# Kernel tuning notes

Hardware: AMD Instinct MI355X
Metric: run time of the kernel (lower is better)

Reference implementation:

```python
import jax, jax.numpy as jnp
import numpy as np

N = 160000          # n_users + n_entities (amazon-book scale)
E = 5_120_000       # nonzeros in A_in (avg degree 32)
DIMS = [64, 64, 32, 16]  # conv_dim_list 64-32-16 on top of embed_dim 64


def setup_inputs() -> dict:
    key = jax.random.key(0)
    ks = jax.random.split(key, 4 + 4 * (len(DIMS) - 1))
    inp = {
        "ego": jax.random.normal(ks[0], (N, DIMS[0]), dtype=jnp.float32) * 0.1,
        "edge_row": jax.random.randint(ks[1], (E,), 0, N, dtype=jnp.int32),
        "edge_col": jax.random.randint(ks[2], (E,), 0, N, dtype=jnp.int32),
        # normalized-adjacency-like values
        "edge_val": jax.random.uniform(ks[3], (E,), dtype=jnp.float32) / 32.0,
    }
    ki = 4
    for i in range(len(DIMS) - 1):
        din, dout = DIMS[i], DIMS[i + 1]
        scale = 1.0 / np.sqrt(din)
        inp[f"W1_{i}"] = jax.random.normal(ks[ki], (din, dout), dtype=jnp.float32) * scale
        inp[f"b1_{i}"] = jnp.zeros((dout,), dtype=jnp.float32)
        inp[f"W2_{i}"] = jax.random.normal(ks[ki + 1], (din, dout), dtype=jnp.float32) * scale
        inp[f"b2_{i}"] = jnp.zeros((dout,), dtype=jnp.float32)
        ki += 2
    return inp


def _leaky(x):
    return jnp.where(x >= 0, x, 0.01 * x)  # nn.LeakyReLU default slope


def _l2norm(x):
    # F.normalize(x, p=2, dim=1), eps=1e-12
    n = jnp.sqrt(jnp.sum(x * x, axis=1, keepdims=True))
    return x / jnp.maximum(n, 1e-12)


def _spmm(row, col, val, x):
    # sparse A_in (COO) @ x : gather neighbor rows, scale, scatter-add
    msgs = val[:, None] * x[col]                      # [E, d]
    return jax.ops.segment_sum(msgs, row, num_segments=N)  # [N, d]


def reference(ego, edge_row, edge_col, edge_val,
              W1_0, b1_0, W2_0, b2_0,
              W1_1, b1_1, W2_1, b2_1,
              W1_2, b1_2, W2_2, b2_2):
    params = [(W1_0, b1_0, W2_0, b2_0),
              (W1_1, b1_1, W2_1, b2_1),
              (W1_2, b1_2, W2_2, b2_2)]
    x = ego
    all_embed = [x]
    for W1, b1, W2, b2 in params:
        side = _spmm(edge_row, edge_col, edge_val, x)         # A_in @ ego
        sum_emb = _leaky((x + side) @ W1 + b1)                # linear1 branch
        bi_emb = _leaky((x * side) @ W2 + b2)                 # linear2 branch
        x = sum_emb + bi_emb                                  # (dropout = identity, eval)
        all_embed.append(_l2norm(x))
    return jnp.concatenate(all_embed, axis=1)                 # [N, 64+64+32+16]
```

## Files before the change

kernel.cpp:

```cpp
#include <hip/hip_runtime.h>
#include <hip/hip_bf16.h>

#define LEAKY(v) ((v) >= 0.0f ? (v) : 0.01f * (v))

typedef int iv4 __attribute__((ext_vector_type(4)));
typedef unsigned short us4 __attribute__((ext_vector_type(4)));
typedef short s8v __attribute__((ext_vector_type(8)));
typedef float f4 __attribute__((ext_vector_type(4)));
typedef float fv8 __attribute__((ext_vector_type(8)));
typedef unsigned uv8 __attribute__((ext_vector_type(8)));

constexpr int SH = 9;
constexpr int RPB = 1 << SH;
constexpr int NBMAX = 320;
constexpr int CHUNK = 6144;

__device__ __forceinline__ unsigned short f2bf(float v) {
  unsigned u = __float_as_uint(v);
  return (unsigned short)((u + 0x7fffu + ((u >> 16) & 1u)) >> 16);
}
__device__ __forceinline__ float bf2f(unsigned short h) {
  return __uint_as_float((unsigned)h << 16);
}

__global__ void k_init(const float* __restrict__ ego, float* __restrict__ out,
                       unsigned short* __restrict__ xh, int n) {
  int tid = blockIdx.x * blockDim.x + threadIdx.x;
  int total = n * 16;
  int stride = gridDim.x * blockDim.x;
  for (int t = tid; t < total; t += stride) {
    int r = t >> 4, c = (t & 15) * 4;
    float4 v = *(const float4*)(ego + (size_t)r * 64 + c);
    *(float4*)(out + (size_t)r * 176 + c) = v;
    if (xh) {
      us4 h;
      h.x = f2bf(v.x); h.y = f2bf(v.y); h.z = f2bf(v.z); h.w = f2bf(v.w);
      *(us4*)(xh + (size_t)r * 64 + c) = h;
    }
  }
}

__global__ void __launch_bounds__(256) k_hist(const int* __restrict__ erow,
                                              int* __restrict__ bcnt, int E, int nb) {
  __shared__ int h[NBMAX];
  for (int i = threadIdx.x; i < NBMAX; i += 256) h[i] = 0;
  __syncthreads();
  int tid = blockIdx.x * blockDim.x + threadIdx.x;
  int stride = gridDim.x * blockDim.x;
  for (int e = tid; e < E; e += stride) atomicAdd(&h[erow[e] >> SH], 1);
  __syncthreads();
  for (int b = threadIdx.x; b < nb; b += 256)
    if (h[b]) atomicAdd(&bcnt[b], h[b]);
}

__global__ void k_scanb(const int* __restrict__ bcnt, int* __restrict__ boff,
                        int* __restrict__ bcur, int* __restrict__ rp,
                        int nb, int n, int E) {
  int l = threadIdx.x;
  constexpr int PB = NBMAX / 64;
  int local[PB];
  int s = 0;
  int base = l * PB;
  for (int j = 0; j < PB; ++j) {
    int b = base + j;
    int c = (b < nb) ? bcnt[b] : 0;
    local[j] = c;
    s += c;
  }
  int incl = s;
  for (int d = 1; d < 64; d <<= 1) {
    int v = __shfl_up(incl, d);
    if (l >= d) incl += v;
  }
  int ex = incl - s;
  for (int j = 0; j < PB; ++j) {
    int b = base + j;
    if (b <= nb) { boff[b] = ex; bcur[b] = ex; }
    ex += local[j];
  }
  if (l == 63) boff[nb] = incl;
  if (l == 0) rp[n] = E;
}

__global__ void __launch_bounds__(256) k_bucket(
    const int* __restrict__ erow, const int* __restrict__ ecol,
    const float* __restrict__ ev, int* __restrict__ bcur,
    int2* __restrict__ bkt, int E, int nb) {
  __shared__ int hist[NBMAX];
  __shared__ int excl[NBMAX + 1];
  __shared__ int curl[NBMAX];
  __shared__ int gbase[NBMAX];
  __shared__ int2 skv[CHUNK];
  int base = blockIdx.x * CHUNK;
  int cnt = min(CHUNK, E - base);

  for (int i = threadIdx.x; i < NBMAX; i += 256) hist[i] = 0;
  __syncthreads();
  for (int i = threadIdx.x; i < cnt; i += 256)
    atomicAdd(&hist[erow[base + i] >> SH], 1);
  __syncthreads();

  if (threadIdx.x < 64) {
    int l = threadIdx.x;
    constexpr int PB = NBMAX / 64;
    int lsum[PB];
    int s = 0;
    for (int j = 0; j < PB; ++j) { lsum[j] = hist[l * PB + j]; s += lsum[j]; }
    int incl = s;
    for (int d = 1; d < 64; d <<= 1) {
      int v = __shfl_up(incl, d);
      if (l >= d) incl += v;
    }
    int ex = incl - s;
    for (int j = 0; j < PB; ++j) { excl[l * PB + j] = ex; ex += lsum[j]; }
    if (l == 63) excl[NBMAX] = incl;
  }
  __syncthreads();

  for (int b = threadIdx.x; b < nb; b += 256) {
    curl[b] = 0;
    int c = hist[b];
    if (c) gbase[b] = atomicAdd(&bcur[b], c);
  }
  __syncthreads();

  for (int i = threadIdx.x; i < cnt; i += 256) {
    int r = erow[base + i];
    int b = r >> SH;
    int lr = r & (RPB - 1);
    int slot = excl[b] + atomicAdd(&curl[b], 1);
    int2 p;
    p.x = (lr << 18) | ecol[base + i];
    p.y = __float_as_int(ev[base + i]);
    skv[slot] = p;
  }
  __syncthreads();

  for (int s = threadIdx.x; s < cnt; s += 256) {
    int lo = 0, hi = nb;
    while (hi - lo > 1) {
      int mid = (lo + hi) >> 1;
      if (excl[mid] <= s) lo = mid; else hi = mid;
    }
    bkt[gbase[lo] + (s - excl[lo])] = skv[s];
  }
}

__global__ void __launch_bounds__(512) k_bsort(
    const int* __restrict__ boff, const int2* __restrict__ bkt,
    int2* __restrict__ cv, int* __restrict__ rp, int n) {
  __shared__ int cnt[RPB];
  __shared__ int sc[RPB];
  __shared__ int exs[RPB];
  __shared__ int cur[RPB];
  int b = blockIdx.x;
  int off = boff[b];
  int m = boff[b + 1] - off;
  int t = threadIdx.x;

  cnt[t] = 0;
  __syncthreads();
  for (int i = t; i < m; i += 512) atomicAdd(&cnt[bkt[off + i].x >> 18], 1);
  __syncthreads();
  sc[t] = cnt[t];
  __syncthreads();
  for (int o = 1; o < RPB; o <<= 1) {
    int v = (t >= o) ? sc[t - o] : 0;
    __syncthreads();
    sc[t] += v;
    __syncthreads();
  }
  int ex = sc[t] - cnt[t];
  exs[t] = ex;
  cur[t] = 0;
  int row = (b << SH) + t;
  if (row < n) rp[row] = off + ex;
  __syncthreads();
  for (int i = t; i < m; i += 512) {
    int2 p = bkt[off + i];
    int lr = p.x >> 18;
    int pos = exs[lr] + atomicAdd(&cur[lr], 1);
    int2 q;
    q.x = p.x & 0x3FFFF;
    q.y = p.y;
    cv[off + pos] = q;
  }
}

template <int DIN, bool BF>
__global__ void __launch_bounds__(256, 8) k_gam(
    const int* __restrict__ rp, const int2* __restrict__ cv,
    const unsigned short* __restrict__ xh, const float* __restrict__ xin,
    unsigned* __restrict__ amp, int n) {
  int row = (int)((blockIdx.x * (unsigned)blockDim.x + threadIdx.x) >> 6);
  int lane = threadIdx.x & 63;
  if (row >= n) return;

  int beg = rp[row], end = rp[row + 1];

  if constexpr (BF) {
    constexpr int LPE = DIN / 8;
    constexpr int EPI = 64 / LPE;
    int eg = lane / LPE;
    int ch = lane % LPE;

    float acc[8];
#pragma unroll
    for (int j = 0; j < 8; ++j) acc[j] = 0.0f;

    if (beg < end) {
      int2 q = cv[min(beg + eg, end - 1)];
      for (int e = beg; e < end; e += EPI) {
        int2 qn = cv[min(e + EPI + eg, end - 1)];
        float val = (e + eg < end) ? __int_as_float(q.y) : 0.0f;
        s8v xr = *(const s8v*)(xh + (size_t)(unsigned)q.x * 64 + ch * 8);
#pragma unroll
        for (int j = 0; j < 4; ++j) {
          unsigned d = ((const unsigned*)&xr)[j];
          acc[2 * j] = fmaf(val, __uint_as_float(d << 16), acc[2 * j]);
          acc[2 * j + 1] = fmaf(val, __uint_as_float(d & 0xffff0000u), acc[2 * j + 1]);
        }
        q = qn;
      }
    }

#pragma unroll
    for (int off = LPE; off < 64; off <<= 1) {
#pragma unroll
      for (int j = 0; j < 8; ++j) acc[j] += __shfl_xor(acc[j], off);
    }

    if (lane < LPE) {
      fv8 xv = *(const fv8*)(xin + (size_t)row * 176 + lane * 8);
      uv8 w;
#pragma unroll
      for (int j = 0; j < 8; ++j) {
        float a = xv[j] + acc[j];
        float m = xv[j] * acc[j];
        w[j] = (unsigned)f2bf(a) | ((unsigned)f2bf(m) << 16);
      }
      *(uv8*)(amp + (size_t)row * 64 + lane * 8) = w;
    }
  } else {
    int f = lane & (DIN - 1);
    float xv = (lane < DIN) ? xin[(size_t)row * 176 + lane] : 0.0f;
    float acc = 0.0f;
    int e = beg;
    if ((e & 1) && e < end) {
      int2 q = cv[e];
      acc = fmaf(__int_as_float(q.y), xin[(size_t)(unsigned)q.x * 176 + f], acc);
      ++e;
    }
    for (; e + 2 <= end; e += 2) {
      iv4 a = *(const iv4*)(cv + e);
      float g0 = xin[(size_t)(unsigned)a.x * 176 + f];
      float g1 = xin[(size_t)(unsigned)a.z * 176 + f];
      acc = fmaf(__int_as_float(a.y), g0, acc);
      acc = fmaf(__int_as_float(a.w), g1, acc);
    }
    if (e < end) {
      int2 q = cv[e];
      acc = fmaf(__int_as_float(q.y), xin[(size_t)(unsigned)q.x * 176 + f], acc);
    }
    if (lane < DIN) {
      float a = xv + acc, m = xv * acc;
      amp[(size_t)row * 64 + lane] = (unsigned)f2bf(a) | ((unsigned)f2bf(m) << 16);
    }
  }
}

template <int DIN, int DOUT>
__global__ void __launch_bounds__(256) k_xf(
    const unsigned* __restrict__ amp,
    const float* __restrict__ W1, const float* __restrict__ b1,
    const float* __restrict__ W2, const float* __restrict__ b2,
    float* __restrict__ outp, unsigned short* __restrict__ xh, int n) {
  constexpr int ROWB = DIN * 2;
  constexpr int RMASK = (ROWB / 16) - 1;
  constexpr int NTC = DOUT / 16;
  __shared__ unsigned short sA[64 * DIN];
  __shared__ unsigned short sM[64 * DIN];
  __shared__ unsigned short sW1[DOUT * DIN];
  __shared__ unsigned short sW2[DOUT * DIN];

  int row0 = blockIdx.x * 64;

  constexpr int PAIRS = DIN / 2;
  for (int i = threadIdx.x; i < 64 * PAIRS; i += 256) {
    int r = i / PAIRS, fp = (i - r * PAIRS) * 2;
    unsigned lo = 0, hi = 0;
    if (row0 + r < n) {
      uint2 q = *(const uint2*)(amp + (size_t)(row0 + r) * 64 + fp);
      lo = (q.x & 0xffffu) | ((q.y & 0xffffu) << 16);
      hi = (q.x >> 16) | (q.y & 0xffff0000u);
    }
    int boff = r * ROWB + ((fp * 2) ^ ((r & RMASK) << 4));
    *(unsigned*)((char*)sA + boff) = lo;
    *(unsigned*)((char*)sM + boff) = hi;
  }
  for (int i = threadIdx.x; i < DIN * DOUT; i += 256) {
    int k = i / DOUT, c = i - k * DOUT;
    int boff = c * ROWB + ((k * 2) ^ ((c & RMASK) << 4));
    *(unsigned short*)((char*)sW1 + boff) = f2bf(W1[i]);
    *(unsigned short*)((char*)sW2 + boff) = f2bf(W2[i]);
  }
  __syncthreads();

  int w = threadIdx.x >> 6, l = threadIdx.x & 63;
  int tr = w;

  f4 acc1[NTC], acc2[NTC];
#pragma unroll
  for (int tc = 0; tc < NTC; ++tc) {
    acc1[tc] = (f4){0.0f, 0.0f, 0.0f, 0.0f};
    acc2[tc] = (f4){0.0f, 0.0f, 0.0f, 0.0f};
  }

#pragma unroll
  for (int k0 = 0; k0 < DIN; k0 += 32) {
    int ra = tr * 16 + (l & 15);
    int inb = (k0 + (l >> 4) * 8) * 2;
    s8v af = *(const s8v*)((const char*)sA + ra * ROWB + (inb ^ ((ra & RMASK) << 4)));
    s8v mf = *(const s8v*)((const char*)sM + ra * ROWB + (inb ^ ((ra & RMASK) << 4)));
#pragma unroll
    for (int tc = 0; tc < NTC; ++tc) {
      int rc = tc * 16 + (l & 15);
      int wb = rc * ROWB + (inb ^ ((rc & RMASK) << 4));
      s8v w1 = *(const s8v*)((const char*)sW1 + wb);
      s8v w2 = *(const s8v*)((const char*)sW2 + wb);
      acc1[tc] = __builtin_amdgcn_mfma_f32_16x16x32_bf16(af, w1, acc1[tc], 0, 0, 0);
      acc2[tc] = __builtin_amdgcn_mfma_f32_16x16x32_bf16(mf, w2, acc2[tc], 0, 0, 0);
    }
  }

#pragma unroll
  for (int tc = 0; tc < NTC; ++tc) {
    int c = tc * 16 + (l & 15);
    float bb1 = b1[c], bb2 = b2[c];
#pragma unroll
    for (int j = 0; j < 4; ++j) {
      int r = tr * 16 + (l >> 4) * 4 + j;
      if (row0 + r < n) {
        float v1 = acc1[tc][j] + bb1;
        float v2 = acc2[tc][j] + bb2;
        float xn = LEAKY(v1) + LEAKY(v2);
        outp[(size_t)(row0 + r) * 176 + c] = xn;
        if (xh) xh[(size_t)(row0 + r) * 64 + c] = f2bf(xn);
      }
    }
  }
}

__global__ void __launch_bounds__(256) k_norm(float* out, int n) {
  int row = (int)((blockIdx.x * (unsigned)blockDim.x + threadIdx.x) >> 6);
  int lane = threadIdx.x & 63;
  if (row >= n) return;
  float* r = out + (size_t)row * 176;
  float a = r[64 + lane];
  float b = (lane < 48) ? r[128 + lane] : 0.0f;
  float sa = a * a;
  float sb_ = (lane < 32) ? b * b : 0.0f;
  float sc = (lane >= 32 && lane < 48) ? b * b : 0.0f;
#pragma unroll
  for (int off = 32; off; off >>= 1) {
    sa += __shfl_xor(sa, off);
    sb_ += __shfl_xor(sb_, off);
    sc += __shfl_xor(sc, off);
  }
  float ia = 1.0f / fmaxf(sqrtf(sa), 1e-12f);
  float ib = 1.0f / fmaxf(sqrtf(sb_), 1e-12f);
  float ic = 1.0f / fmaxf(sqrtf(sc), 1e-12f);
  r[64 + lane] = a * ia;
  if (lane < 48) r[128 + lane] = b * ((lane < 32) ? ib : ic);
}

extern "C" void kernel_launch(void* const* d_in, const int* in_sizes, int n_in,
                              void* d_out, int out_size, void* d_ws, size_t ws_size,
                              hipStream_t stream) {
  const float* ego = (const float*)d_in[0];
  const int* erow = (const int*)d_in[1];
  const int* ecol = (const int*)d_in[2];
  const float* ev = (const float*)d_in[3];
  const int n = in_sizes[0] / 64;
  const int E = in_sizes[1];
  const int nb = (n + RPB - 1) >> SH;

  float* out = (float*)d_out;

  int2* bkt = (int2*)d_ws;
  int2* cv = bkt + E;
  int* rp = (int*)(cv + E);
  int* bcnt = rp + n + 1;
  int* boff = bcnt + NBMAX;
  int* bcur = boff + NBMAX + 1;
  unsigned short* xh = (unsigned short*)(bcur + NBMAX);
  unsigned* amp = (unsigned*)d_ws;

  size_t need_bf = (size_t)((char*)(xh + (size_t)n * 64) - (char*)d_ws);
  bool bf = ws_size >= need_bf;
  unsigned short* xhp = bf ? xh : nullptr;

  const int rblocks = (n + 3) / 4;
  const int xblocks = (n + 63) / 64;

  k_init<<<2048, 256, 0, stream>>>(ego, out, xhp, n);
  hipMemsetAsync(bcnt, 0, NBMAX * sizeof(int), stream);
  k_hist<<<1024, 256, 0, stream>>>(erow, bcnt, E, nb);
  k_scanb<<<1, 64, 0, stream>>>(bcnt, boff, bcur, rp, nb, n, E);
  k_bucket<<<(E + CHUNK - 1) / CHUNK, 256, 0, stream>>>(erow, ecol, ev, bcur, bkt, E, nb);
  k_bsort<<<nb, 512, 0, stream>>>(boff, bkt, cv, rp, n);

  const float* W1_0 = (const float*)d_in[4];
  const float* B1_0 = (const float*)d_in[5];
  const float* W2_0 = (const float*)d_in[6];
  const float* B2_0 = (const float*)d_in[7];
  const float* W1_1 = (const float*)d_in[8];
  const float* B1_1 = (const float*)d_in[9];
  const float* W2_1 = (const float*)d_in[10];
  const float* B2_1 = (const float*)d_in[11];
  const float* W1_2 = (const float*)d_in[12];
  const float* B1_2 = (const float*)d_in[13];
  const float* W2_2 = (const float*)d_in[14];
  const float* B2_2 = (const float*)d_in[15];

  if (bf) {
    k_gam<64, true><<<rblocks, 256, 0, stream>>>(rp, cv, xh, out, amp, n);
    k_xf<64, 64><<<xblocks, 256, 0, stream>>>(amp, W1_0, B1_0, W2_0, B2_0, out + 64, xh, n);
    k_gam<64, true><<<rblocks, 256, 0, stream>>>(rp, cv, xh, out + 64, amp, n);
    k_xf<64, 32><<<xblocks, 256, 0, stream>>>(amp, W1_1, B1_1, W2_1, B2_1, out + 128, xh, n);
    k_gam<32, true><<<rblocks, 256, 0, stream>>>(rp, cv, xh, out + 128, amp, n);
    k_xf<32, 16><<<xblocks, 256, 0, stream>>>(amp, W1_2, B1_2, W2_2, B2_2, out + 160, nullptr, n);
  } else {
    k_gam<64, false><<<rblocks, 256, 0, stream>>>(rp, cv, nullptr, out, amp, n);
    k_xf<64, 64><<<xblocks, 256, 0, stream>>>(amp, W1_0, B1_0, W2_0, B2_0, out + 64, nullptr, n);
    k_gam<64, false><<<rblocks, 256, 0, stream>>>(rp, cv, nullptr, out + 64, amp, n);
    k_xf<64, 32><<<xblocks, 256, 0, stream>>>(amp, W1_1, B1_1, W2_1, B2_1, out + 128, nullptr, n);
    k_gam<32, false><<<rblocks, 256, 0, stream>>>(rp, cv, nullptr, out + 128, amp, n);
    k_xf<32, 16><<<xblocks, 256, 0, stream>>>(amp, W1_2, B1_2, W2_2, B2_2, out + 160, nullptr, n);
  }

  k_norm<<<rblocks, 256, 0, stream>>>(out, n);
}
```

Baseline: 759.5 us.

## Fuse sparse gather-aggregate with dense MFMA transform into one per-layer kernel

Merges the gather/aggregate kernel and the MFMA linear-transform kernel into one kernel per layer. Each 64-row block has its four waves aggregate 16 rows apiece, writing the bf16 sum and product straight into shared memory, which removes the global amp intermediate round-trip. The bf16 activation buffer is now ping-ponged between two workspace regions (one overlapping the bucket area), and the fp32 fallback path is dropped. The trade-off is lower occupancy (launch bound 5) and serialized per-wave row loops, which may hide gather latency less well.

```diff
diff --git a/kernel.cpp b/kernel.cpp
--- a/kernel.cpp
+++ b/kernel.cpp
@@ -7,8 +7,6 @@
 typedef unsigned short us4 __attribute__((ext_vector_type(4)));
 typedef short s8v __attribute__((ext_vector_type(8)));
 typedef float f4 __attribute__((ext_vector_type(4)));
-typedef float fv8 __attribute__((ext_vector_type(8)));
-typedef unsigned uv8 __attribute__((ext_vector_type(8)));
 
 constexpr int SH = 9;
 constexpr int RPB = 1 << SH;
@@ -18,9 +16,6 @@
 __device__ __forceinline__ unsigned short f2bf(float v) {
   unsigned u = __float_as_uint(v);
   return (unsigned short)((u + 0x7fffu + ((u >> 16) & 1u)) >> 16);
-}
-__device__ __forceinline__ float bf2f(unsigned short h) {
-  return __uint_as_float((unsigned)h << 16);
 }
 
 __global__ void k_init(const float* __restrict__ ego, float* __restrict__ out,
@@ -32,11 +27,9 @@
     int r = t >> 4, c = (t & 15) * 4;
     float4 v = *(const float4*)(ego + (size_t)r * 64 + c);
     *(float4*)(out + (size_t)r * 176 + c) = v;
-    if (xh) {
-      us4 h;
-      h.x = f2bf(v.x); h.y = f2bf(v.y); h.z = f2bf(v.z); h.w = f2bf(v.w);
-      *(us4*)(xh + (size_t)r * 64 + c) = h;
-    }
+    us4 h;
+    h.x = f2bf(v.x); h.y = f2bf(v.y); h.z = f2bf(v.z); h.w = f2bf(v.w);
+    *(us4*)(xh + (size_t)r * 64 + c) = h;
   }
 }
 
@@ -187,33 +180,51 @@
   }
 }
 
-template <int DIN, bool BF>
-__global__ void __launch_bounds__(256, 8) k_gam(
+template <int DIN, int DOUT>
+__global__ void __launch_bounds__(256, 5) k_fgx(
     const int* __restrict__ rp, const int2* __restrict__ cv,
-    const unsigned short* __restrict__ xh, const float* __restrict__ xin,
-    unsigned* __restrict__ amp, int n) {
-  int row = (int)((blockIdx.x * (unsigned)blockDim.x + threadIdx.x) >> 6);
-  int lane = threadIdx.x & 63;
-  if (row >= n) return;
-
-  int beg = rp[row], end = rp[row + 1];
-
-  if constexpr (BF) {
-    constexpr int LPE = DIN / 8;
-    constexpr int EPI = 64 / LPE;
-    int eg = lane / LPE;
-    int ch = lane % LPE;
+    const unsigned short* __restrict__ xhin, const float* __restrict__ xin,
+    const float* __restrict__ W1, const float* __restrict__ b1,
+    const float* __restrict__ W2, const float* __restrict__ b2,
+    float* __restrict__ outp, unsigned short* __restrict__ xhout, int n) {
+  constexpr int ROWB = DIN * 2;
+  constexpr int RMASK = (ROWB / 16) - 1;
+  constexpr int NTC = DOUT / 16;
+  constexpr int LPE = DIN / 8;
+  constexpr int EPI = 64 / LPE;
+  __shared__ unsigned short sA[64 * DIN];
+  __shared__ unsigned short sM[64 * DIN];
+  __shared__ unsigned short sW1[DOUT * DIN];
+  __shared__ unsigned short sW2[DOUT * DIN];
+
+  int tid = threadIdx.x;
+  int w = tid >> 6, lane = tid & 63;
+  int row0 = blockIdx.x * 64;
+
+  for (int i = tid; i < DIN * DOUT; i += 256) {
+    int k = i / DOUT, c = i - k * DOUT;
+    int boffb = c * ROWB + ((k * 2) ^ ((c & RMASK) << 4));
+    *(unsigned short*)((char*)sW1 + boffb) = f2bf(W1[i]);
+    *(unsigned short*)((char*)sW2 + boffb) = f2bf(W2[i]);
+  }
+
+  int g = lane / LPE, ch = lane % LPE;
+  for (int rr = 0; rr < 16; ++rr) {
+    int lr = w * 16 + rr;
+    int row = row0 + lr;
+    if (row >= n) break;
+    int beg = rp[row], end = rp[row + 1];
 
     float acc[8];
 #pragma unroll
     for (int j = 0; j < 8; ++j) acc[j] = 0.0f;
 
     if (beg < end) {
-      int2 q = cv[min(beg + eg, end - 1)];
+      int2 q = cv[min(beg + g, end - 1)];
       for (int e = beg; e < end; e += EPI) {
-        int2 qn = cv[min(e + EPI + eg, end - 1)];
-        float val = (e + eg < end) ? __int_as_float(q.y) : 0.0f;
-        s8v xr = *(const s8v*)(xh + (size_t)(unsigned)q.x * 64 + ch * 8);
+        int2 qn = cv[min(e + EPI + g, end - 1)];
+        float val = (e + g < end) ? __int_as_float(q.y) : 0.0f;
+        s8v xr = *(const s8v*)(xhin + (size_t)(unsigned)q.x * 64 + ch * 8);
 #pragma unroll
         for (int j = 0; j < 4; ++j) {
           unsigned d = ((const unsigned*)&xr)[j];
@@ -223,7 +234,6 @@
         q = qn;
       }
     }
-
 #pragma unroll
     for (int off = LPE; off < 64; off <<= 1) {
 #pragma unroll
@@ -231,82 +241,25 @@
     }
 
     if (lane < LPE) {
-      fv8 xv = *(const fv8*)(xin + (size_t)row * 176 + lane * 8);
-      uv8 w;
-#pragma unroll
-      for (int j = 0; j < 8; ++j) {
-        float a = xv[j] + acc[j];
-        float m = xv[j] * acc[j];
-        w[j] = (unsigned)f2bf(a) | ((unsigned)f2bf(m) << 16);
+      float4 x0 = *(const float4*)(xin + (size_t)row * 176 + ch * 8);
+      float4 x1 = *(const float4*)(xin + (size_t)row * 176 + ch * 8 + 4);
+      float xa[8] = {x0.x, x0.y, x0.z, x0.w, x1.x, x1.y, x1.z, x1.w};
+      unsigned aw[4], mw[4];
+#pragma unroll
+      for (int j = 0; j < 4; ++j) {
+        float a0 = xa[2 * j] + acc[2 * j], a1 = xa[2 * j + 1] + acc[2 * j + 1];
+        float m0 = xa[2 * j] * acc[2 * j], m1 = xa[2 * j + 1] * acc[2 * j + 1];
+        aw[j] = (unsigned)f2bf(a0) | ((unsigned)f2bf(a1) << 16);
+        mw[j] = (unsigned)f2bf(m0) | ((unsigned)f2bf(m1) << 16);
       }
-      *(uv8*)(amp + (size_t)row * 64 + lane * 8) = w;
-    }
-  } else {
-    int f = lane & (DIN - 1);
-    float xv = (lane < DIN) ? xin[(size_t)row * 176 + lane] : 0.0f;
-    float acc = 0.0f;
-    int e = beg;
-    if ((e & 1) && e < end) {
-      int2 q = cv[e];
-      acc = fmaf(__int_as_float(q.y), xin[(size_t)(unsigned)q.x * 176 + f], acc);
-      ++e;
-    }
-    for (; e + 2 <= end; e += 2) {
-      iv4 a = *(const iv4*)(cv + e);
-      float g0 = xin[(size_t)(unsigned)a.x * 176 + f];
-      float g1 = xin[(size_t)(unsigned)a.z * 176 + f];
-      acc = fmaf(__int_as_float(a.y), g0, acc);
-      acc = fmaf(__int_as_float(a.w), g1, acc);
-    }
-    if (e < end) {
-      int2 q = cv[e];
-      acc = fmaf(__int_as_float(q.y), xin[(size_t)(unsigned)q.x * 176 + f], acc);
-    }
-    if (lane < DIN) {
-      float a = xv + acc, m = xv * acc;
-      amp[(size_t)row * 64 + lane] = (unsigned)f2bf(a) | ((unsigned)f2bf(m) << 16);
-    }
-  }
-}
-
-template <int DIN, int DOUT>
-__global__ void __launch_bounds__(256) k_xf(
-    const unsigned* __restrict__ amp,
-    const float* __restrict__ W1, const float* __restrict__ b1,
-    const float* __restrict__ W2, const float* __restrict__ b2,
-    float* __restrict__ outp, unsigned short* __restrict__ xh, int n) {
-  constexpr int ROWB = DIN * 2;
-  constexpr int RMASK = (ROWB / 16) - 1;
-  constexpr int NTC = DOUT / 16;
-  __shared__ unsigned short sA[64 * DIN];
-  __shared__ unsigned short sM[64 * DIN];
-  __shared__ unsigned short sW1[DOUT * DIN];
-  __shared__ unsigned short sW2[DOUT * DIN];
-
-  int row0 = blockIdx.x * 64;
-
-  constexpr int PAIRS = DIN / 2;
-  for (int i = threadIdx.x; i < 64 * PAIRS; i += 256) {
-    int r = i / PAIRS, fp = (i - r * PAIRS) * 2;
-    unsigned lo = 0, hi = 0;
-    if (row0 + r < n) {
-      uint2 q = *(const uint2*)(amp + (size_t)(row0 + r) * 64 + fp);
-      lo = (q.x & 0xffffu) | ((q.y & 0xffffu) << 16);
-      hi = (q.x >> 16) | (q.y & 0xffff0000u);
-    }
-    int boff = r * ROWB + ((fp * 2) ^ ((r & RMASK) << 4));
-    *(unsigned*)((char*)sA + boff) = lo;
-    *(unsigned*)((char*)sM + boff) = hi;
-  }
-  for (int i = threadIdx.x; i < DIN * DOUT; i += 256) {
-    int k = i / DOUT, c = i - k * DOUT;
-    int boff = c * ROWB + ((k * 2) ^ ((c & RMASK) << 4));
-    *(unsigned short*)((char*)sW1 + boff) = f2bf(W1[i]);
-    *(unsigned short*)((char*)sW2 + boff) = f2bf(W2[i]);
-  }
-  __syncthreads();
-
-  int w = threadIdx.x >> 6, l = threadIdx.x & 63;
+      int boffb = lr * ROWB + ((ch * 16) ^ ((lr & RMASK) << 4));
+      *(iv4*)((char*)sA + boffb) = (iv4){(int)aw[0], (int)aw[1], (int)aw[2], (int)aw[3]};
+      *(iv4*)((char*)sM + boffb) = (iv4){(int)mw[0], (int)mw[1], (int)mw[2], (int)mw[3]};
+    }
+  }
+  __syncthreads();
+
+  int l = lane;
   int tr = w;
 
   f4 acc1[NTC], acc2[NTC];
@@ -345,7 +298,7 @@
         float v2 = acc2[tc][j] + bb2;
         float xn = LEAKY(v1) + LEAKY(v2);
         outp[(size_t)(row0 + r) * 176 + c] = xn;
-        if (xh) xh[(size_t)(row0 + r) * 64 + c] = f2bf(xn);
+        if (xhout) xhout[(size_t)(row0 + r) * 64 + c] = f2bf(xn);
       }
     }
   }
@@ -393,17 +346,13 @@
   int* bcnt = rp + n + 1;
   int* boff = bcnt + NBMAX;
   int* bcur = boff + NBMAX + 1;
-  unsigned short* xh = (unsigned short*)(bcur + NBMAX);
-  unsigned* amp = (unsigned*)d_ws;
-
-  size_t need_bf = (size_t)((char*)(xh + (size_t)n * 64) - (char*)d_ws);
-  bool bf = ws_size >= need_bf;
-  unsigned short* xhp = bf ? xh : nullptr;
+  unsigned short* xh_b = (unsigned short*)(bcur + NBMAX);
+  unsigned short* xh_a = (unsigned short*)d_ws;
 
   const int rblocks = (n + 3) / 4;
   const int xblocks = (n + 63) / 64;
 
-  k_init<<<2048, 256, 0, stream>>>(ego, out, xhp, n);
+  k_init<<<2048, 256, 0, stream>>>(ego, out, xh_b, n);
   hipMemsetAsync(bcnt, 0, NBMAX * sizeof(int), stream);
   k_hist<<<1024, 256, 0, stream>>>(erow, bcnt, E, nb);
   k_scanb<<<1, 64, 0, stream>>>(bcnt, boff, bcur, rp, nb, n, E);
@@ -423,21 +372,12 @@
   const float* W2_2 = (const float*)d_in[14];
   const float* B2_2 = (const float*)d_in[15];
 
-  if (bf) {
-    k_gam<64, true><<<rblocks, 256, 0, stream>>>(rp, cv, xh, out, amp, n);
-    k_xf<64, 64><<<xblocks, 256, 0, stream>>>(amp, W1_0, B1_0, W2_0, B2_0, out + 64, xh, n);
-    k_gam<64, true><<<rblocks, 256, 0, stream>>>(rp, cv, xh, out + 64, amp, n);
-    k_xf<64, 32><<<xblocks, 256, 0, stream>>>(amp, W1_1, B1_1, W2_1, B2_1, out + 128, xh, n);
-    k_gam<32, true><<<rblocks, 256, 0, stream>>>(rp, cv, xh, out + 128, amp, n);
-    k_xf<32, 16><<<xblocks, 256, 0, stream>>>(amp, W1_2, B1_2, W2_2, B2_2, out + 160, nullptr, n);
-  } else {
-    k_gam<64, false><<<rblocks, 256, 0, stream>>>(rp, cv, nullptr, out, amp, n);
-    k_xf<64, 64><<<xblocks, 256, 0, stream>>>(amp, W1_0, B1_0, W2_0, B2_0, out + 64, nullptr, n);
-    k_gam<64, false><<<rblocks, 256, 0, stream>>>(rp, cv, nullptr, out + 64, amp, n);
-    k_xf<64, 32><<<xblocks, 256, 0, stream>>>(amp, W1_1, B1_1, W2_1, B2_1, out + 128, nullptr, n);
-    k_gam<32, false><<<rblocks, 256, 0, stream>>>(rp, cv, nullptr, out + 128, amp, n);
-    k_xf<32, 16><<<xblocks, 256, 0, stream>>>(amp, W1_2, B1_2, W2_2, B2_2, out + 160, nullptr, n);
-  }
+  k_fgx<64, 64><<<xblocks, 256, 0, stream>>>(
+      rp, cv, xh_b, out, W1_0, B1_0, W2_0, B2_0, out + 64, xh_a, n);
+  k_fgx<64, 32><<<xblocks, 256, 0, stream>>>(
+      rp, cv, xh_a, out + 64, W1_1, B1_1, W2_1, B2_1, out + 128, xh_b, n);
+  k_fgx<32, 16><<<xblocks, 256, 0, stream>>>(
+      rp, cv, xh_b, out + 128, W1_2, B1_2, W2_2, B2_2, out + 160, nullptr, n);
 
   k_norm<<<rblocks, 256, 0, stream>>>(out, n);
 }
```

New measurement: 790.8 us. 1.04x slower.
